# Kernel optimization log

Measured on AMD Instinct MI355X. Metric: run time of the kernel, lower is better.

The kernel has to match this reference:

```python
import jax, jax.numpy as jnp
import numpy as np

B, S, D, F, E, K = 2, 2048, 1024, 4096, 8, 2


def setup_inputs() -> dict:
    key = jax.random.key(0)
    ks = jax.random.split(key, 6)
    s = 0.02  # init scale
    return {
        "x": jax.random.normal(ks[0], (B, S, D), dtype=jnp.float32),
        "Wr": jax.random.normal(ks[1], (D, E), dtype=jnp.float32) * s,
        "br": jnp.zeros((E,), dtype=jnp.float32),
        "W1": jax.random.normal(ks[2], (E, D, F), dtype=jnp.float32) * s,
        "b1": jnp.zeros((E, F), dtype=jnp.float32),
        "W2": jax.random.normal(ks[3], (E, F, D), dtype=jnp.float32) * s,
        "b2": jnp.zeros((E, D), dtype=jnp.float32),
        "top_k": K,
    }


def reference(x, Wr, br, W1, b1, W2, b2, top_k):
    b, s, d = x.shape
    e = Wr.shape[1]
    xt = x.reshape(-1, d)                              # [T, D], T = b*s
    logits = xt @ Wr + br                              # [T, E]
    probs = jax.nn.softmax(logits, axis=-1)            # [T, E] router probabilities
    topw, topi = jax.lax.top_k(probs, top_k)           # [T, K] each
    # combine weight per (token, expert): weight if expert in token's top-k else 0
    cw = jnp.sum(jax.nn.one_hot(topi, e, dtype=x.dtype) * topw[..., None], axis=1)  # [T, E]
    # dense grouped FFN: every expert over every token, then weighted combine
    h = jax.nn.relu(jnp.einsum('td,edf->tef', xt, W1) + b1)   # [T, E, F]
    y = jnp.einsum('tef,efd->ted', h, W2) + b2                # [T, E, D]
    out = jnp.einsum('te,ted->td', cw, y).reshape(b, s, d)    # [B, S, D]
    return out, probs.reshape(b, s, e)
```

## Files before the change

### kernel.cpp

```cpp
#include <hip/hip_runtime.h>
#include <hip/hip_bf16.h>


#define T_TOK 4096
#define D_DIM 1024
#define F_DIM 4096
#define E_NUM 8
#define CAP_ROWS 9216
#define N_TILES (CAP_ROWS/128)
#define PGRID 512

typedef __attribute__((ext_vector_type(8))) short short8v;
typedef __attribute__((ext_vector_type(8))) unsigned short ushort8v;
typedef __attribute__((ext_vector_type(4))) float f32x4;

static __device__ __forceinline__ unsigned short f2bf(float f){
  union { float f; unsigned u; } v; v.f = f;
  unsigned r = (v.u + 0x7fffu + ((v.u >> 16) & 1u)) >> 16;
  return (unsigned short)r;
}
static __device__ __forceinline__ float bf2f(unsigned short s){
  union { unsigned u; float f; } v; v.u = ((unsigned)s) << 16;
  return v.f;
}

static __device__ __forceinline__ void gload16(const void* g, void* l) {
  __builtin_amdgcn_global_load_lds(
      (const __attribute__((address_space(1))) unsigned int*)g,
      (__attribute__((address_space(3))) unsigned int*)l, 16, 0, 0);
}

__global__ __launch_bounds__(256) void k_router(
    const float* __restrict__ x, const float* __restrict__ Wr,
    const float* __restrict__ br, float* __restrict__ probs_out,
    int* __restrict__ topi, float* __restrict__ topw, int* __restrict__ counts,
    unsigned short* __restrict__ xbf)
{
  const int lane = threadIdx.x & 63;
  const int t = blockIdx.x * 4 + (threadIdx.x >> 6);
  float xv[16];
  #pragma unroll
  for (int i = 0; i < 16; ++i) xv[i] = x[(size_t)t*D_DIM + i*64 + lane];
  #pragma unroll
  for (int i = 0; i < 16; ++i) xbf[(size_t)t*D_DIM + i*64 + lane] = f2bf(xv[i]);
  float pe[E_NUM];
  #pragma unroll
  for (int e = 0; e < E_NUM; ++e) {
    float p = 0.f;
    #pragma unroll
    for (int i = 0; i < 16; ++i) p += xv[i] * Wr[(i*64 + lane)*E_NUM + e];
    #pragma unroll
    for (int off = 32; off >= 1; off >>= 1) p += __shfl_xor(p, off);
    pe[e] = p + br[e];
  }
  float m = pe[0];
  #pragma unroll
  for (int e = 1; e < E_NUM; ++e) m = fmaxf(m, pe[e]);
  float s = 0.f;
  #pragma unroll
  for (int e = 0; e < E_NUM; ++e) { pe[e] = expf(pe[e] - m); s += pe[e]; }
  const float inv = 1.f / s;
  int e1 = 0; float v1 = pe[0];
  #pragma unroll
  for (int e = 1; e < E_NUM; ++e) if (pe[e] > v1) { v1 = pe[e]; e1 = e; }
  int e2 = (e1 == 0) ? 1 : 0; float v2 = pe[e2];
  #pragma unroll
  for (int e = 0; e < E_NUM; ++e) if (e != e1 && pe[e] > v2) { v2 = pe[e]; e2 = e; }
  if (lane == 0) {
    #pragma unroll
    for (int e = 0; e < E_NUM; ++e) probs_out[(size_t)t*E_NUM + e] = pe[e] * inv;
    topi[t*2+0] = e1; topw[t*2+0] = v1 * inv;
    topi[t*2+1] = e2; topw[t*2+1] = v2 * inv;
    atomicAdd(&counts[e1], 1);
    atomicAdd(&counts[e2], 1);
  }
}

__global__ __launch_bounds__(256) void k_assign(
    const int* __restrict__ counts,
    const int* __restrict__ topi, const float* __restrict__ topw,
    int* __restrict__ cursor,
    int* __restrict__ rows_token, float* __restrict__ rows_w,
    int* __restrict__ pair_of, int* __restrict__ tile_e)
{
  __shared__ int base_s[E_NUM + 1];
  if (threadIdx.x == 0) {
    int base = 0;
    #pragma unroll
    for (int e = 0; e < E_NUM; ++e) {
      base_s[e] = base;
      base += ((counts[e] + 127) >> 7) << 7;
    }
    base_s[E_NUM] = base;
  }
  __syncthreads();
  if (blockIdx.x == 0 && threadIdx.x < N_TILES) {
    const int r0 = threadIdx.x << 7;
    int e = -1;
    #pragma unroll
    for (int k = 0; k < E_NUM; ++k)
      if (r0 >= base_s[k] && r0 < base_s[k+1]) e = k;
    tile_e[threadIdx.x] = e;
  }
  const int t = blockIdx.x * 256 + threadIdx.x;
  if (t < T_TOK) {
    #pragma unroll
    for (int k = 0; k < 2; ++k) {
      const int e = topi[t*2+k];
      const int slot = atomicAdd(&cursor[e], 1);
      const int pid = base_s[e] + slot;
      rows_token[pid] = t;
      rows_w[pid] = topw[t*2+k];
      pair_of[t*2+k] = pid;
    }
  }
}

template<int R, int C>
__global__ __launch_bounds__(256) void k_tcvt(const float* __restrict__ in,
                                              unsigned short* __restrict__ out)
{
  const size_t eo = (size_t)blockIdx.z * R * C;
  const int r0 = blockIdx.y * 64, c0 = blockIdx.x * 64;
  __shared__ unsigned short ls[64][66];
  const int t = threadIdx.x;
  const int rr = t >> 4, cc = (t & 15) * 4;
  #pragma unroll
  for (int p = 0; p < 4; ++p) {
    const float4 v = *(const float4*)&in[eo + (size_t)(r0 + p*16 + rr)*C + c0 + cc];
    ls[p*16+rr][cc+0]=f2bf(v.x); ls[p*16+rr][cc+1]=f2bf(v.y);
    ls[p*16+rr][cc+2]=f2bf(v.z); ls[p*16+rr][cc+3]=f2bf(v.w);
  }
  __syncthreads();
  const int kc = (t & 7) * 8, nn0 = t >> 3;
  #pragma unroll
  for (int p = 0; p < 2; ++p) {
    const int nn = nn0 + p*32;
    ushort8v o;
    #pragma unroll
    for (int j = 0; j < 8; ++j) o[j] = ls[kc + j][nn];
    *(ushort8v*)&out[eo + (size_t)(c0 + nn)*R + r0 + kc] = o;
  }
}

template<bool GATHER, int NDIM, int KFULL, int EPI>
__global__ __launch_bounds__(256, 2) void k_gemm(
    const unsigned short* __restrict__ A,
    const unsigned short* __restrict__ Bt,
    const float* __restrict__ bias,
    const int* __restrict__ tile_e,
    const int* __restrict__ rows_token,
    const float* __restrict__ rows_w,
    unsigned short* __restrict__ outp,
    int tot, int nbx, int nkt, int kch)
{
  const int q = blockIdx.x & 7;
  const int bslot = blockIdx.x >> 3;
  const int region = tot >> 3;
  const int cpq = region / N_TILES;
  __shared__ __align__(16) unsigned short LB[2][256 * 64];
  const int tid = threadIdx.x;
  const int lane = tid & 63;
  const int w = tid >> 6;
  const int lr = lane >> 3;
  const int g  = (lane & 7) ^ lr;
  unsigned lbase[8];
  if (w < 2) {
    #pragma unroll
    for (int i = 0; i < 8; ++i) lbase[i] = (unsigned)((w*64 + i*8) * 64);
  } else {
    #pragma unroll
    for (int i = 0; i < 8; ++i) lbase[i] = (unsigned)((128*64) + ((w-2)*64 + i*8) * 64);
  }
  const int wr = w >> 1, wc = w & 1;
  const int cl = lane & 15, rgb = lane >> 4;
  const int sz = cl & 7;

  for (int tw = bslot; tw < region; tw += (PGRID >> 3)) {
    const int combo = q * cpq + tw / N_TILES;
    const int by = tw % N_TILES;
    const int bx = combo % nbx;
    const int z  = combo / nbx;
    const int e = tile_e[by];
    if (e < 0) continue;
    const int rt = by * 128;
    const int ntc = bx * 128;
    const int koff = z * kch;
    const unsigned short* gp[8];
    if (w < 2) {
      #pragma unroll
      for (int i = 0; i < 8; ++i) {
        const int rl = w*64 + i*8 + lr;
        const int rowidx = GATHER ? rows_token[rt + rl] : (rt + rl);
        gp[i] = A + (size_t)rowidx * KFULL + koff + g*8;
      }
    } else {
      const unsigned short* Be = Bt + (size_t)e * NDIM * KFULL;
      #pragma unroll
      for (int i = 0; i < 8; ++i) {
        const int rl = (w-2)*64 + i*8 + lr;
        gp[i] = Be + (size_t)(ntc + rl) * KFULL + koff + g*8;
      }
    }
    f32x4 acc[4][4] = {};

    #define STG8(tt, bb)                                          \
      { const int _ko = (tt) * 64;                                \
        _Pragma("unroll")                                         \
        for (int _i = 0; _i < 8; ++_i)                            \
          gload16(gp[_i] + _ko, &LB[bb][lbase[_i]]); }

    STG8(0, 0)
    asm volatile("s_waitcnt vmcnt(0)" ::: "memory");
    __builtin_amdgcn_s_barrier();

    for (int t = 0; t < nkt; ++t) {
      const int bb = t & 1;
      if (t + 1 < nkt) STG8(t+1, bb^1)
      const unsigned short* Sb = &LB[bb][0];
      short8v a[4][2], b[4][2];
      #pragma unroll
      for (int m = 0; m < 4; ++m) {
        a[m][0] = *(const short8v*)&Sb[(wr*64 + m*16 + cl)*64 + ((0*4+rgb)^sz)*8];
        a[m][1] = *(const short8v*)&Sb[(wr*64 + m*16 + cl)*64 + ((1*4+rgb)^sz)*8];
      }
      #pragma unroll
      for (int n = 0; n < 4; ++n) {
        b[n][0] = *(const short8v*)&Sb[(128*64) + (wc*64 + n*16 + cl)*64 + ((0*4+rgb)^sz)*8];
        b[n][1] = *(const short8v*)&Sb[(128*64) + (wc*64 + n*16 + cl)*64 + ((1*4+rgb)^sz)*8];
      }
      __builtin_amdgcn_s_setprio(1);
      #pragma unroll
      for (int m = 0; m < 4; ++m)
        #pragma unroll
        for (int n = 0; n < 4; ++n) {
          acc[m][n] = __builtin_amdgcn_mfma_f32_16x16x32_bf16(a[m][0], b[n][0], acc[m][n], 0, 0, 0);
          acc[m][n] = __builtin_amdgcn_mfma_f32_16x16x32_bf16(a[m][1], b[n][1], acc[m][n], 0, 0, 0);
        }
      __builtin_amdgcn_s_setprio(0);
      asm volatile("s_waitcnt vmcnt(0)" ::: "memory");
      __builtin_amdgcn_s_barrier();
    }
    #undef STG8

    unsigned short* op = outp;
    if (EPI == 2) op += (size_t)z * CAP_ROWS * NDIM;
    const bool addb = (EPI == 1) || (z == 0);
    const size_t ebias = (size_t)e * NDIM;
    #pragma unroll
    for (int m = 0; m < 4; ++m) {
      const int row = rt + wr*64 + m*16 + rgb*4;
      float4 rw4 = make_float4(0,0,0,0);
      if (EPI == 2) rw4 = *(const float4*)&rows_w[row];
      #pragma unroll
      for (int n = 0; n < 4; ++n) {
        const int col = ntc + wc*64 + n*16 + cl;
        const float bv = addb ? bias[ebias + col] : 0.f;
        #pragma unroll
        for (int r = 0; r < 4; ++r) {
          float v = acc[m][n][r] + bv;
          if (EPI == 1) v = fmaxf(v, 0.f);
          else          v *= ((const float*)&rw4)[r];
          const unsigned short hb = f2bf(v);
          const unsigned short ob = (unsigned short)__shfl_xor((int)(unsigned)hb, 1);
          if ((lane & 1) == 0) {
            const unsigned pk = (unsigned)hb | ((unsigned)ob << 16);
            *(unsigned*)&op[(size_t)(row + r)*NDIM + col] = pk;
          }
        }
      }
    }
  }
}

__global__ __launch_bounds__(256) void k_combine(
    const unsigned short* __restrict__ yp, const int* __restrict__ pair_of,
    float* __restrict__ out, int ksplit)
{
  const int gid = blockIdx.x * 256 + threadIdx.x;
  const int t = gid >> 7;
  const int c = (gid & 127) * 8;
  float o[8] = {0,0,0,0,0,0,0,0};
  #pragma unroll
  for (int k = 0; k < 2; ++k) {
    const int p = pair_of[t*2+k];
    for (int s = 0; s < ksplit; ++s) {
      const ushort8v v = *(const ushort8v*)&yp[((size_t)s*CAP_ROWS + p)*D_DIM + c];
      #pragma unroll
      for (int j = 0; j < 8; ++j) o[j] += bf2f(v[j]);
    }
  }
  float4 o0; o0.x=o[0]; o0.y=o[1]; o0.z=o[2]; o0.w=o[3];
  float4 o1; o1.x=o[4]; o1.y=o[5]; o1.z=o[6]; o1.w=o[7];
  *(float4*)&out[(size_t)t*D_DIM + c]     = o0;
  *(float4*)&out[(size_t)t*D_DIM + c + 4] = o1;
}

extern "C" void kernel_launch(void* const* d_in, const int* in_sizes, int n_in,
                              void* d_out, int out_size, void* d_ws, size_t ws_size,
                              hipStream_t stream)
{
  const float* x  = (const float*)d_in[0];
  const float* Wr = (const float*)d_in[1];
  const float* br = (const float*)d_in[2];
  const float* W1 = (const float*)d_in[3];
  const float* b1 = (const float*)d_in[4];
  const float* W2 = (const float*)d_in[5];
  const float* b2 = (const float*)d_in[6];
  (void)in_sizes; (void)n_in; (void)out_size;

  float* out   = (float*)d_out;
  float* probs = out + (size_t)T_TOK * D_DIM;

  char* w = (char*)d_ws;
  size_t off = 0;
  int*   counts     = (int*)(w + off); off += 256;
  int*   cursor     = (int*)(w + off); off += 256;
  int*   rows_token = (int*)(w + off); off += (size_t)CAP_ROWS*4;
  float* rows_w     = (float*)(w + off); off += (size_t)CAP_ROWS*4;
  const size_t zbytes = off;
  int*   tile_e     = (int*)(w + off); off += 3072;
  int*   topi       = (int*)(w + off); off += (size_t)T_TOK*2*4;
  float* topw       = (float*)(w + off); off += (size_t)T_TOK*2*4;
  int*   pair_of    = (int*)(w + off); off += (size_t)T_TOK*2*4;
  off = (off + 255) & ~(size_t)255;
  unsigned short* xbf = (unsigned short*)(w + off); off += (size_t)T_TOK*D_DIM*2;
  unsigned short* Wt  = (unsigned short*)(w + off); off += (size_t)E_NUM*D_DIM*F_DIM*2;
  unsigned short* h   = (unsigned short*)(w + off); off += (size_t)CAP_ROWS*F_DIM*2;
  unsigned short* yp  = (unsigned short*)(w + off);
  const size_t ypart_bytes = (size_t)CAP_ROWS * D_DIM * 2;
  const int ksplit = (ws_size >= off + 2 * ypart_bytes) ? 2 : 1;
  const int kch2 = F_DIM / ksplit;
  const int nkt2 = kch2 / 64;

  hipMemsetAsync(d_ws, 0, zbytes, stream);
  k_router<<<T_TOK / 4, 256, 0, stream>>>(x, Wr, br, probs, topi, topw, counts, xbf);
  k_assign<<<T_TOK / 256, 256, 0, stream>>>(counts, topi, topw, cursor,
                                            rows_token, rows_w, pair_of, tile_e);
  k_tcvt<D_DIM, F_DIM><<<dim3(F_DIM/64, D_DIM/64, E_NUM), 256, 0, stream>>>(W1, Wt);
  k_gemm<true, F_DIM, D_DIM, 1><<<PGRID, 256, 0, stream>>>(
      xbf, Wt, b1, tile_e, rows_token, rows_w, h,
      (F_DIM/128)*N_TILES, F_DIM/128, D_DIM/64, D_DIM);
  k_tcvt<F_DIM, D_DIM><<<dim3(D_DIM/64, F_DIM/64, E_NUM), 256, 0, stream>>>(W2, Wt);
  k_gemm<false, D_DIM, F_DIM, 2><<<PGRID, 256, 0, stream>>>(
      h, Wt, b2, tile_e, rows_token, rows_w, yp,
      (D_DIM/128)*N_TILES*ksplit, D_DIM/128, nkt2, kch2);
  k_combine<<<T_TOK * D_DIM / 8 / 256, 256, 0, stream>>>(yp, pair_of, out, ksplit);
}
```

Measured before the change: 452.1 us.

## Replace static tile mapping with atomic work queue and drop split-K in second GEMM

Both grouped GEMMs now pull tiles from a global atomic counter instead of using a fixed XCD-striped static assignment, which balances work when padded tiles are skipped. The second GEMM no longer splits K across two partial outputs, so it writes one y buffer and the combine kernel reads two rows instead of up to four. This removes the extra partial buffer traffic and the extra adds, but the second GEMM has half as many tiles with twice the K length, which may reduce parallelism. Each tile fetch also adds an atomic and two block barriers.

```diff
diff --git a/kernel.cpp b/kernel.cpp
--- a/kernel.cpp
+++ b/kernel.cpp
@@ -152,13 +152,10 @@
     const int* __restrict__ rows_token,
     const float* __restrict__ rows_w,
     unsigned short* __restrict__ outp,
-    int tot, int nbx, int nkt, int kch)
-{
-  const int q = blockIdx.x & 7;
-  const int bslot = blockIdx.x >> 3;
-  const int region = tot >> 3;
-  const int cpq = region / N_TILES;
+    int* __restrict__ tileq, int tot, int nkt)
+{
   __shared__ __align__(16) unsigned short LB[2][256 * 64];
+  __shared__ int tile_s;
   const int tid = threadIdx.x;
   const int lane = tid & 63;
   const int w = tid >> 6;
@@ -176,30 +173,32 @@
   const int cl = lane & 15, rgb = lane >> 4;
   const int sz = cl & 7;
 
-  for (int tw = bslot; tw < region; tw += (PGRID >> 3)) {
-    const int combo = q * cpq + tw / N_TILES;
-    const int by = tw % N_TILES;
-    const int bx = combo % nbx;
-    const int z  = combo / nbx;
+  for (;;) {
+    if (tid == 0) tile_s = atomicAdd(tileq, 1);
+    __syncthreads();
+    const int idx = tile_s;
+    __syncthreads();
+    if (idx >= tot) break;
+    const int bx = idx / N_TILES;
+    const int by = idx - bx * N_TILES;
     const int e = tile_e[by];
     if (e < 0) continue;
     const int rt = by * 128;
     const int ntc = bx * 128;
-    const int koff = z * kch;
     const unsigned short* gp[8];
     if (w < 2) {
       #pragma unroll
       for (int i = 0; i < 8; ++i) {
         const int rl = w*64 + i*8 + lr;
         const int rowidx = GATHER ? rows_token[rt + rl] : (rt + rl);
-        gp[i] = A + (size_t)rowidx * KFULL + koff + g*8;
+        gp[i] = A + (size_t)rowidx * KFULL + g*8;
       }
     } else {
       const unsigned short* Be = Bt + (size_t)e * NDIM * KFULL;
       #pragma unroll
       for (int i = 0; i < 8; ++i) {
         const int rl = (w-2)*64 + i*8 + lr;
-        gp[i] = Be + (size_t)(ntc + rl) * KFULL + koff + g*8;
+        gp[i] = Be + (size_t)(ntc + rl) * KFULL + g*8;
       }
     }
     f32x4 acc[4][4] = {};
@@ -243,9 +242,6 @@
     }
     #undef STG8
 
-    unsigned short* op = outp;
-    if (EPI == 2) op += (size_t)z * CAP_ROWS * NDIM;
-    const bool addb = (EPI == 1) || (z == 0);
     const size_t ebias = (size_t)e * NDIM;
     #pragma unroll
     for (int m = 0; m < 4; ++m) {
@@ -255,7 +251,7 @@
       #pragma unroll
       for (int n = 0; n < 4; ++n) {
         const int col = ntc + wc*64 + n*16 + cl;
-        const float bv = addb ? bias[ebias + col] : 0.f;
+        const float bv = bias[ebias + col];
         #pragma unroll
         for (int r = 0; r < 4; ++r) {
           float v = acc[m][n][r] + bv;
@@ -265,7 +261,7 @@
           const unsigned short ob = (unsigned short)__shfl_xor((int)(unsigned)hb, 1);
           if ((lane & 1) == 0) {
             const unsigned pk = (unsigned)hb | ((unsigned)ob << 16);
-            *(unsigned*)&op[(size_t)(row + r)*NDIM + col] = pk;
+            *(unsigned*)&outp[(size_t)(row + r)*NDIM + col] = pk;
           }
         }
       }
@@ -274,22 +270,19 @@
 }
 
 __global__ __launch_bounds__(256) void k_combine(
-    const unsigned short* __restrict__ yp, const int* __restrict__ pair_of,
-    float* __restrict__ out, int ksplit)
+    const unsigned short* __restrict__ y, const int* __restrict__ pair_of,
+    float* __restrict__ out)
 {
   const int gid = blockIdx.x * 256 + threadIdx.x;
   const int t = gid >> 7;
   const int c = (gid & 127) * 8;
-  float o[8] = {0,0,0,0,0,0,0,0};
-  #pragma unroll
-  for (int k = 0; k < 2; ++k) {
-    const int p = pair_of[t*2+k];
-    for (int s = 0; s < ksplit; ++s) {
-      const ushort8v v = *(const ushort8v*)&yp[((size_t)s*CAP_ROWS + p)*D_DIM + c];
-      #pragma unroll
-      for (int j = 0; j < 8; ++j) o[j] += bf2f(v[j]);
-    }
-  }
+  const int p0 = pair_of[t*2+0];
+  const int p1 = pair_of[t*2+1];
+  const ushort8v a = *(const ushort8v*)&y[(size_t)p0*D_DIM + c];
+  const ushort8v b = *(const ushort8v*)&y[(size_t)p1*D_DIM + c];
+  float o[8];
+  #pragma unroll
+  for (int j = 0; j < 8; ++j) o[j] = bf2f(a[j]) + bf2f(b[j]);
   float4 o0; o0.x=o[0]; o0.y=o[1]; o0.z=o[2]; o0.w=o[3];
   float4 o1; o1.x=o[4]; o1.y=o[5]; o1.z=o[6]; o1.w=o[7];
   *(float4*)&out[(size_t)t*D_DIM + c]     = o0;
@@ -307,7 +300,7 @@
   const float* b1 = (const float*)d_in[4];
   const float* W2 = (const float*)d_in[5];
   const float* b2 = (const float*)d_in[6];
-  (void)in_sizes; (void)n_in; (void)out_size;
+  (void)in_sizes; (void)n_in; (void)out_size; (void)ws_size;
 
   float* out   = (float*)d_out;
   float* probs = out + (size_t)T_TOK * D_DIM;
@@ -316,6 +309,7 @@
   size_t off = 0;
   int*   counts     = (int*)(w + off); off += 256;
   int*   cursor     = (int*)(w + off); off += 256;
+  int*   tileq      = (int*)(w + off); off += 256;
   int*   rows_token = (int*)(w + off); off += (size_t)CAP_ROWS*4;
   float* rows_w     = (float*)(w + off); off += (size_t)CAP_ROWS*4;
   const size_t zbytes = off;
@@ -327,11 +321,7 @@
   unsigned short* xbf = (unsigned short*)(w + off); off += (size_t)T_TOK*D_DIM*2;
   unsigned short* Wt  = (unsigned short*)(w + off); off += (size_t)E_NUM*D_DIM*F_DIM*2;
   unsigned short* h   = (unsigned short*)(w + off); off += (size_t)CAP_ROWS*F_DIM*2;
-  unsigned short* yp  = (unsigned short*)(w + off);
-  const size_t ypart_bytes = (size_t)CAP_ROWS * D_DIM * 2;
-  const int ksplit = (ws_size >= off + 2 * ypart_bytes) ? 2 : 1;
-  const int kch2 = F_DIM / ksplit;
-  const int nkt2 = kch2 / 64;
+  unsigned short* y   = (unsigned short*)(w + off); off += (size_t)CAP_ROWS*D_DIM*2;
 
   hipMemsetAsync(d_ws, 0, zbytes, stream);
   k_router<<<T_TOK / 4, 256, 0, stream>>>(x, Wr, br, probs, topi, topw, counts, xbf);
@@ -340,10 +330,10 @@
   k_tcvt<D_DIM, F_DIM><<<dim3(F_DIM/64, D_DIM/64, E_NUM), 256, 0, stream>>>(W1, Wt);
   k_gemm<true, F_DIM, D_DIM, 1><<<PGRID, 256, 0, stream>>>(
       xbf, Wt, b1, tile_e, rows_token, rows_w, h,
-      (F_DIM/128)*N_TILES, F_DIM/128, D_DIM/64, D_DIM);
+      &tileq[0], (F_DIM/128)*N_TILES, D_DIM/64);
   k_tcvt<F_DIM, D_DIM><<<dim3(D_DIM/64, F_DIM/64, E_NUM), 256, 0, stream>>>(W2, Wt);
   k_gemm<false, D_DIM, F_DIM, 2><<<PGRID, 256, 0, stream>>>(
-      h, Wt, b2, tile_e, rows_token, rows_w, yp,
-      (D_DIM/128)*N_TILES*ksplit, D_DIM/128, nkt2, kch2);
-  k_combine<<<T_TOK * D_DIM / 8 / 256, 256, 0, stream>>>(yp, pair_of, out, ksplit);
-}
+      h, Wt, b2, tile_e, rows_token, rows_w, y,
+      &tileq[32], (D_DIM/128)*N_TILES, F_DIM/64);
+  k_combine<<<T_TOK * D_DIM / 8 / 256, 256, 0, stream>>>(y, pair_of, out);
+}
```

Result: slower. 495.4 us (+9.6%).
